# Kernel tuning notes

Measured on AMD Instinct MI355X. Metric: run time of the kernel, lower is better.

The kernel has to match this reference:

```python
import jax, jax.numpy as jnp
import numpy as np

D_MODEL = 256
D_STATE = 64
NGROUPS = 2
EXPAND = 4
HEADDIM = 128
D_CONV = 4
D_INNER = EXPAND * D_MODEL              # 1024
NHEADS = D_INNER // HEADDIM             # 8
GN = NGROUPS * D_STATE                  # 128
D_IN_PROJ = 2 * D_INNER + 2 * GN + NHEADS  # 2312
EPS = 1e-5


def setup_inputs() -> dict:
    key = jax.random.key(0)
    ks = jax.random.split(key, 12)
    B, L = 2, 4096
    u = jax.random.normal(ks[0], (B, L, D_MODEL), dtype=jnp.float32)
    ln_gamma = jnp.ones((D_MODEL,), jnp.float32)
    ln_beta = jnp.zeros((D_MODEL,), jnp.float32)
    W_in = jax.random.normal(ks[1], (D_MODEL, D_IN_PROJ), jnp.float32) / np.sqrt(D_MODEL)
    conv_w = jax.random.normal(ks[2], (D_INNER + 2 * GN, D_CONV), jnp.float32) * 0.2
    conv_b = jax.random.normal(ks[3], (D_INNER + 2 * GN,), jnp.float32) * 0.02
    dt_bias = jnp.log(jnp.expm1(jax.random.uniform(ks[4], (NHEADS,), jnp.float32, 0.001, 0.1)))
    A_log = jnp.log(jax.random.uniform(ks[5], (NHEADS,), jnp.float32, 1.0, 16.0))
    D_param = jnp.ones((NHEADS,), jnp.float32)
    B_head_scale = jnp.ones((NHEADS, GN), jnp.float32) + 0.02 * jax.random.normal(ks[6], (NHEADS, GN), jnp.float32)
    rms_weight = jnp.ones((D_INNER,), jnp.float32)
    W_out = jax.random.normal(ks[7], (D_INNER, D_MODEL), jnp.float32) / np.sqrt(D_INNER)
    return dict(u=u, ln_gamma=ln_gamma, ln_beta=ln_beta, W_in=W_in, conv_w=conv_w,
                conv_b=conv_b, dt_bias=dt_bias, A_log=A_log, D_param=D_param,
                B_head_scale=B_head_scale, rms_weight=rms_weight, W_out=W_out)


def _mamba_mes(xn, W_in, conv_w, conv_b, dt_bias, A_log, D_param, B_head_scale, rms_weight, W_out):
    B, L, _ = xn.shape
    H, P, K = NHEADS, HEADDIM, D_CONV
    zxbcdt = xn @ W_in                                   # (B,L,2312)
    z = zxbcdt[..., :D_INNER]
    xBC = zxbcdt[..., D_INNER:D_INNER + D_INNER + 2 * GN]
    dt = zxbcdt[..., -H:]
    dt_pos = jax.nn.softplus(dt + dt_bias)               # (B,L,H)
    # causal depthwise conv1d + silu
    xp = jnp.pad(xBC, ((0, 0), (K - 1, 0), (0, 0)))
    conv = sum(xp[:, k:k + L, :] * conv_w[:, k] for k in range(K)) + conv_b
    xBC = jax.nn.silu(conv)
    x = xBC[..., :D_INNER]
    B_shared = xBC[..., D_INNER:D_INNER + GN]            # (B,L,GN)
    C_shared = xBC[..., D_INNER + GN:]                   # (B,L,GN)
    # MES: per-head B via diagonal scale, shared x (mean over heads) and shared C
    B_h = B_shared[:, :, None, :] * B_head_scale[None, None]          # (B,L,H,GN)
    x_shared = x.reshape(B, L, H, P).mean(axis=2)                     # (B,L,P)
    A = -jnp.exp(A_log)                                               # (H,)
    dA = jnp.exp(dt_pos * A)                                          # (B,L,H)
    # selective scan; per-head state (GN, P)
    def step(state, inp):
        dA_t, dt_t, B_t, C_t, x_t = inp   # (B,H),(B,H),(B,H,GN),(B,GN),(B,P)
        state = dA_t[:, :, None, None] * state + jnp.einsum('bh,bhn,bp->bhnp', dt_t, B_t, x_t)
        y_t = jnp.einsum('bn,bhnp->bhp', C_t, state)
        return state, y_t
    init = jnp.zeros((B, H, GN, P), xn.dtype)
    xs = (jnp.moveaxis(dA, 1, 0), jnp.moveaxis(dt_pos, 1, 0), jnp.moveaxis(B_h, 1, 0),
          jnp.moveaxis(C_shared, 1, 0), jnp.moveaxis(x_shared, 1, 0))
    _, ys = jax.lax.scan(step, init, xs)
    y = jnp.moveaxis(ys, 0, 1)                                        # (B,L,H,P)
    y = y + D_param[None, None, :, None] * x_shared[:, :, None, :]    # skip term D*x
    y = y.reshape(B, L, D_INNER)
    # gated RMSNorm: y * silu(z), then rmsnorm
    yg = y * jax.nn.silu(z)
    y = yg * jax.lax.rsqrt(jnp.mean(yg * yg, axis=-1, keepdims=True) + EPS) * rms_weight
    return y @ W_out


def reference(u, ln_gamma, ln_beta, W_in, conv_w, conv_b, dt_bias, A_log,
              D_param, B_head_scale, rms_weight, W_out):
    # pre-LayerNorm
    mu = jnp.mean(u, axis=-1, keepdims=True)
    var = jnp.mean((u - mu) ** 2, axis=-1, keepdims=True)
    xn = (u - mu) * jax.lax.rsqrt(var + EPS) * ln_gamma + ln_beta
    out = _mamba_mes(xn, W_in, conv_w, conv_b, dt_bias, A_log, D_param,
                     B_head_scale, rms_weight, W_out)
    return u + out  # dropout is identity in eval
```

## Files before the change

### kernel.cpp

```cpp
#include <hip/hip_runtime.h>
#include <math.h>

#define LN_TOK 4096
#define NB 2
#define NROWS (NB * LN_TOK)
#define DMODEL 256
#define DINNER 1024
#define NHEADS 8
#define GNN 128
#define DPROJ 2312
#define ZSTRIDE 2432
#define EPSF 1e-5f
#define NCHUNK 32
#define CHUNK 128
#define APAD 72
#define BPAD 64
#define MPAD 136
#define TT 16

typedef unsigned short u16;
typedef unsigned int u32;
typedef __attribute__((ext_vector_type(8))) short shortx8;
typedef __attribute__((ext_vector_type(4))) float floatx4;

__device__ __forceinline__ float sigmoidf_(float v) { return 1.f / (1.f + __expf(-v)); }
__device__ __forceinline__ float siluf_(float v)    { return v / (1.f + __expf(-v)); }
__device__ __forceinline__ float softplusf_(float v){ return v > 20.f ? v : log1pf(__expf(v)); }
__device__ __forceinline__ float b2f(u16 h) { return __uint_as_float(((u32)h) << 16); }
__device__ __forceinline__ u16 f2b(float f) {
    u32 u = __float_as_uint(f);
    u32 r = (u + 0x7fffu + ((u >> 16) & 1u)) >> 16;
    return (u16)r;
}
__device__ __forceinline__ void gld16(const void* g, void* l) {
    __builtin_amdgcn_global_load_lds((const __attribute__((address_space(1))) unsigned int*)g,
                                     (__attribute__((address_space(3))) unsigned int*)l, 16, 0, 0);
}

__global__ __launch_bounds__(256) void k_prologue(const float* __restrict__ u,
                                                  const float* __restrict__ gam,
                                                  const float* __restrict__ bet,
                                                  u16* __restrict__ xn,
                                                  const float* __restrict__ W_in,
                                                  u16* __restrict__ Wt,
                                                  const float* __restrict__ W_out,
                                                  u16* __restrict__ Wot) {
    __shared__ float smem[64 * 65];
    int bid = blockIdx.x;
    int tid = threadIdx.x;
    if (bid < NROWS) {
        float v = u[(size_t)bid * DMODEL + tid];
        float* s1 = smem;
        float* s2 = smem + 256;
        s1[tid] = v; s2[tid] = v * v;
        __syncthreads();
        for (int off = 128; off > 0; off >>= 1) {
            if (tid < off) { s1[tid] += s1[tid + off]; s2[tid] += s2[tid + off]; }
            __syncthreads();
        }
        float mean = s1[0] * (1.f / DMODEL);
        float var  = s2[0] * (1.f / DMODEL) - mean * mean;
        float r = rsqrtf(var + EPSF);
        xn[(size_t)bid * DMODEL + tid] = f2b((v - mean) * r * gam[tid] + bet[tid]);
    } else {
        const float* in; u16* outp; int R, C, Cp, gx, gy;
        if (bid < NROWS + 152) {
            int q = bid - NROWS;
            in = W_in; outp = Wt; R = DMODEL; C = DPROJ; Cp = ZSTRIDE;
            gx = q % (ZSTRIDE / 64); gy = q / (ZSTRIDE / 64);
        } else {
            int q = bid - NROWS - 152;
            in = W_out; outp = Wot; R = DINNER; C = DMODEL; Cp = DMODEL;
            gx = q % (DMODEL / 64); gy = q / (DMODEL / 64);
        }
        float (*tile)[65] = (float(*)[65])smem;
        int c0 = gx * 64, r0 = gy * 64;
        int tx = tid & 63, ty = tid >> 6;
        for (int rr = ty; rr < 64; rr += 4) {
            int r = r0 + rr, c = c0 + tx;
            tile[rr][tx] = (r < R && c < C) ? in[(size_t)r * C + c] : 0.f;
        }
        __syncthreads();
        for (int cc = ty; cc < 64; cc += 4) {
            int c = c0 + cc, r = r0 + tx;
            if (c < Cp && r < R) outp[(size_t)c * R + r] = f2b(tile[tx][cc]);
        }
    }
}

__global__ __launch_bounds__(256) void k_gemm_bf(const u16* __restrict__ A,
                                                 const u16* __restrict__ Bt,
                                                 u16* __restrict__ C,
                                                 int K, int ldc) {
    __shared__ u16 As[128 * BPAD];
    __shared__ u16 Bs[128 * BPAD];
    int tid = threadIdx.x;
    int wave = tid >> 6, lane = tid & 63;
    int wm = wave >> 1, wn = wave & 1;
    int quad = lane >> 4, l16 = lane & 15;
    int m0 = blockIdx.y * 128, n0 = blockIdx.x * 128;
    floatx4 acc[4][4] = {};
    for (int k0 = 0; k0 < K; k0 += 64) {
#pragma unroll
        for (int p = 0; p < 4; p++) {
            int i = p * 256 + tid;
            int row = i >> 3, kk = (i & 7) << 3;
            gld16(&A[(size_t)(m0 + row) * K + k0 + kk], &As[i * 8]);
            gld16(&Bt[(size_t)(n0 + row) * K + k0 + kk], &Bs[i * 8]);
        }
        __syncthreads();
#pragma unroll
        for (int ks = 0; ks < 64; ks += 32) {
            shortx8 af[4], bfr[4];
#pragma unroll
            for (int i = 0; i < 4; i++)
                af[i] = *(shortx8*)&As[(wm * 64 + i * 16 + l16) * BPAD + ks + (quad << 3)];
#pragma unroll
            for (int j = 0; j < 4; j++)
                bfr[j] = *(shortx8*)&Bs[(wn * 64 + j * 16 + l16) * BPAD + ks + (quad << 3)];
#pragma unroll
            for (int i = 0; i < 4; i++)
#pragma unroll
                for (int j = 0; j < 4; j++)
                    acc[i][j] = __builtin_amdgcn_mfma_f32_16x16x32_bf16(af[i], bfr[j], acc[i][j], 0, 0, 0);
        }
        __syncthreads();
    }
#pragma unroll
    for (int i = 0; i < 4; i++) {
        int row = m0 + wm * 64 + i * 16 + quad * 4;
#pragma unroll
        for (int j = 0; j < 4; j++) {
            int col = n0 + wn * 64 + j * 16 + l16;
#pragma unroll
            for (int r = 0; r < 4; r++)
                C[(size_t)(row + r) * ldc + col] = f2b(acc[i][j][r]);
        }
    }
}

__global__ __launch_bounds__(256) void k_gemm2(const u16* __restrict__ A,
                                               const u16* __restrict__ Bt,
                                               float* __restrict__ C,
                                               int K, int ldc,
                                               const float* __restrict__ addC) {
    __shared__ u16 As[128 * BPAD];
    __shared__ u16 Bs[64 * BPAD];
    int tid = threadIdx.x;
    int wave = tid >> 6, lane = tid & 63;
    int wm = wave >> 1, wn = wave & 1;
    int quad = lane >> 4, l16 = lane & 15;
    int m0 = blockIdx.y * 128, n0 = blockIdx.x * 64;
    floatx4 acc[4][2] = {};
    for (int k0 = 0; k0 < K; k0 += 64) {
#pragma unroll
        for (int p = 0; p < 4; p++) {
            int i = p * 256 + tid;
            int row = i >> 3, kk = (i & 7) << 3;
            gld16(&A[(size_t)(m0 + row) * K + k0 + kk], &As[i * 8]);
        }
#pragma unroll
        for (int p = 0; p < 2; p++) {
            int i = p * 256 + tid;
            int row = i >> 3, kk = (i & 7) << 3;
            gld16(&Bt[(size_t)(n0 + row) * K + k0 + kk], &Bs[i * 8]);
        }
        __syncthreads();
#pragma unroll
        for (int ks = 0; ks < 64; ks += 32) {
            shortx8 af[4], bfr[2];
#pragma unroll
            for (int i = 0; i < 4; i++)
                af[i] = *(shortx8*)&As[(wm * 64 + i * 16 + l16) * BPAD + ks + (quad << 3)];
#pragma unroll
            for (int j = 0; j < 2; j++)
                bfr[j] = *(shortx8*)&Bs[(wn * 32 + j * 16 + l16) * BPAD + ks + (quad << 3)];
#pragma unroll
            for (int i = 0; i < 4; i++)
#pragma unroll
                for (int j = 0; j < 2; j++)
                    acc[i][j] = __builtin_amdgcn_mfma_f32_16x16x32_bf16(af[i], bfr[j], acc[i][j], 0, 0, 0);
        }
        __syncthreads();
    }
#pragma unroll
    for (int i = 0; i < 4; i++) {
        int row = m0 + wm * 64 + i * 16 + quad * 4;
#pragma unroll
        for (int j = 0; j < 2; j++) {
            int col = n0 + wn * 32 + j * 16 + l16;
#pragma unroll
            for (int r = 0; r < 4; r++) {
                size_t idx = (size_t)(row + r) * ldc + col;
                float v = acc[i][j][r];
                if (addC) v += addC[idx];
                C[idx] = v;
            }
        }
    }
}

#define LDW 1296
__global__ __launch_bounds__(256) void k_conv(const u16* __restrict__ zxb,
                                              const float* __restrict__ cw,
                                              const float* __restrict__ cb,
                                              const float* __restrict__ dt_bias,
                                              const float* __restrict__ A_log,
                                              u16* __restrict__ xsh, u16* __restrict__ Bsh,
                                              u16* __restrict__ Csh, u16* __restrict__ XT,
                                              u16* __restrict__ BT,
                                              float* __restrict__ dtp, float* __restrict__ laa) {
    int blk = blockIdx.x;
    int b = blk / (LN_TOK / TT), tile = blk % (LN_TOK / TT);
    int t0 = tile * TT;
    int tid = threadIdx.x;
    __shared__ u16 ld[(TT + 3) * LDW];
    __shared__ float sv[TT][260];
    __shared__ u16 bcv[TT][132];

    for (int i = tid; i < (TT + 3) * 161; i += 256) {
        int r = i / 161, ch = (i % 161) * 8;
        int t = t0 - 3 + r;
        int4 v = make_int4(0, 0, 0, 0);
        if (t >= 0)
            v = *(const int4*)&zxb[((size_t)(b * LN_TOK + t)) * ZSTRIDE + DINNER + ch];
        *(int4*)&ld[r * LDW + ch] = v;
    }

    int cmap[5];
#pragma unroll
    for (int k = 0; k < 4; k++) cmap[k] = (tid >> 7) * 512 + (tid & 127) + 128 * k;
    cmap[4] = 1024 + tid;
    float w0[5], w1[5], w2[5], w3[5], bias[5];
#pragma unroll
    for (int k = 0; k < 5; k++) {
        int c = cmap[k];
        w0[k] = cw[c * 4 + 0]; w1[k] = cw[c * 4 + 1];
        w2[k] = cw[c * 4 + 2]; w3[k] = cw[c * 4 + 3];
        bias[k] = cb[c];
    }
    float dtb = 0.f, negA = 0.f;
    if (tid < NHEADS) { dtb = dt_bias[tid]; negA = -__expf(A_log[tid]); }

    __syncthreads();

    float h1[5], h2[5], h3[5];
#pragma unroll
    for (int k = 0; k < 5; k++) {
        h3[k] = b2f(ld[0 * LDW + cmap[k]]);
        h2[k] = b2f(ld[1 * LDW + cmap[k]]);
        h1[k] = b2f(ld[2 * LDW + cmap[k]]);
    }

    for (int m = 0; m < TT; m++) {
        int t = t0 + m;
        size_t rowp = (size_t)(b * LN_TOK + t) * GNN;
        float xpart = 0.f;
#pragma unroll
        for (int k = 0; k < 5; k++) {
            float cur = b2f(ld[(m + 3) * LDW + cmap[k]]);
            float conv = bias[k] + w3[k] * cur + w2[k] * h1[k] + w1[k] * h2[k] + w0[k] * h3[k];
            h3[k] = h2[k]; h2[k] = h1[k]; h1[k] = cur;
            float s = siluf_(conv);
            if (k < 4) xpart += s;
            else {
                u16 sb = f2b(s);
                if (tid < 128) { Bsh[rowp + tid] = sb; bcv[m][tid] = sb; }
                else           Csh[rowp + tid - 128] = sb;
            }
        }
        sv[m][tid] = xpart;
        if (tid < NHEADS) {
            float dtv = b2f(ld[(m + 3) * LDW + 1280 + tid]) + dtb;
            float dp = softplusf_(dtv);
            size_t idx = ((size_t)(b * NHEADS + tid)) * LN_TOK + t;
            dtp[idx] = dp;
            laa[idx] = negA * dp;
        }
    }
    __syncthreads();

    for (int idx = tid; idx < TT * 128; idx += 256) {
        int m = idx >> 7, p = idx & 127;
        xsh[(size_t)(b * LN_TOK + t0 + m) * GNN + p] =
            f2b((sv[m][p] + sv[m][p + 128]) * 0.125f);
    }
    {
        int p = tid & 127, tg = tid >> 7;
        u16 ox[8], ob[8];
#pragma unroll
        for (int j = 0; j < 8; j++) {
            int m = tg * 8 + j;
            ox[j] = f2b((sv[m][p] + sv[m][p + 128]) * 0.125f);
            ob[j] = bcv[m][p];
        }
        size_t base = ((size_t)(b * GNN + p)) * LN_TOK + t0 + tg * 8;
        int4 vx = make_int4((u32)ox[0] | ((u32)ox[1] << 16), (u32)ox[2] | ((u32)ox[3] << 16),
                            (u32)ox[4] | ((u32)ox[5] << 16), (u32)ox[6] | ((u32)ox[7] << 16));
        int4 vb = make_int4((u32)ob[0] | ((u32)ob[1] << 16), (u32)ob[2] | ((u32)ob[3] << 16),
                            (u32)ob[4] | ((u32)ob[5] << 16), (u32)ob[6] | ((u32)ob[7] << 16));
        *(int4*)&XT[base] = vx;
        *(int4*)&BT[base] = vb;
    }
}

__global__ __launch_bounds__(256) void k_chunkS(const u16* __restrict__ BT,
                                                const u16* __restrict__ XT,
                                                const float* __restrict__ scale,
                                                const float* __restrict__ laa,
                                                const float* __restrict__ dtp,
                                                u16* __restrict__ states,
                                                float* __restrict__ gtot) {
    int blk = blockIdx.x;
    int c = blk & 31, h = (blk >> 5) & 7, b = blk >> 8;
    int t0 = c * CHUNK;
    __shared__ u16 As[128 * APAD];
    __shared__ u16 Bs[128 * APAD];
    __shared__ float g[128], esc[128], scl[128];
    int tid = threadIdx.x;
    int wave = tid >> 6, lane = tid & 63;
    int wm = wave >> 1, wn = wave & 1;
    int quad = lane >> 4, l16 = lane & 15;
    size_t bhbase = (size_t)(b * NHEADS + h) * LN_TOK + t0;
    if (tid < 128) g[tid] = laa[bhbase + tid];
    __syncthreads();
#pragma unroll
    for (int off = 1; off < 128; off <<= 1) {
        float v = 0.f;
        if (tid < 128 && tid >= off) v = g[tid - off];
        __syncthreads();
        if (tid < 128) g[tid] += v;
        __syncthreads();
    }
    if (tid < 128) {
        esc[tid] = __expf(g[127] - g[tid]) * dtp[bhbase + tid];
        scl[tid] = scale[h * GNN + tid];
    }
    if (tid == 0) gtot[(size_t)(b * NHEADS + h) * NCHUNK + c] = g[127];
    __syncthreads();
    floatx4 acc[4][4] = {};
    size_t tbase = (size_t)(b * GNN) * LN_TOK + t0;
    for (int k0 = 0; k0 < 128; k0 += 64) {
#pragma unroll
        for (int p = 0; p < 4; p++) {
            int i = p * 256 + tid;
            int row = i >> 3, kk = (i & 7) << 3;
            int4 raw = *(const int4*)&BT[tbase + (size_t)row * LN_TOK + k0 + kk];
            u16* rp = (u16*)&raw;
            float sr = scl[row];
            u32 w[4];
#pragma unroll
            for (int q = 0; q < 4; q++) {
                u16 a  = f2b(b2f(rp[2 * q])     * sr * esc[k0 + kk + 2 * q]);
                u16 bb = f2b(b2f(rp[2 * q + 1]) * sr * esc[k0 + kk + 2 * q + 1]);
                w[q] = (u32)a | ((u32)bb << 16);
            }
            *(int4*)&As[row * APAD + kk] = make_int4(w[0], w[1], w[2], w[3]);
            *(int4*)&Bs[row * APAD + kk] = *(const int4*)&XT[tbase + (size_t)row * LN_TOK + k0 + kk];
        }
        __syncthreads();
#pragma unroll
        for (int ks = 0; ks < 64; ks += 32) {
            shortx8 af[4], bfr[4];
#pragma unroll
            for (int i = 0; i < 4; i++)
                af[i] = *(shortx8*)&As[(wm * 64 + i * 16 + l16) * APAD + ks + (quad << 3)];
#pragma unroll
            for (int j = 0; j < 4; j++)
                bfr[j] = *(shortx8*)&Bs[(wn * 64 + j * 16 + l16) * APAD + ks + (quad << 3)];
#pragma unroll
            for (int i = 0; i < 4; i++)
#pragma unroll
                for (int j = 0; j < 4; j++)
                    acc[i][j] = __builtin_amdgcn_mfma_f32_16x16x32_bf16(af[i], bfr[j], acc[i][j], 0, 0, 0);
        }
        __syncthreads();
    }
    size_t sbase = (size_t)blk * 16384;
#pragma unroll
    for (int i = 0; i < 4; i++) {
        int n0 = wm * 64 + i * 16 + quad * 4;
#pragma unroll
        for (int j = 0; j < 4; j++) {
            int p = wn * 64 + j * 16 + l16;
            u16 o[4];
#pragma unroll
            for (int r = 0; r < 4; r++) o[r] = f2b(acc[i][j][r]);
            u32 lo = (u32)o[0] | ((u32)o[1] << 16);
            u32 hi = (u32)o[2] | ((u32)o[3] << 16);
            *(uint2*)&states[sbase + (size_t)p * CHUNK + n0] = make_uint2(lo, hi);
        }
    }
}

__global__ void k_scan(u16* __restrict__ states, const float* __restrict__ gtot) {
    int idx = blockIdx.x * 256 + threadIdx.x;
    int bh = idx >> 13;
    int np = (idx & 8191) * 2;
    __shared__ float sG[NCHUNK];
    if (threadIdx.x < NCHUNK) sG[threadIdx.x] = __expf(gtot[bh * NCHUNK + threadIdx.x]);
    __syncthreads();
    size_t base = (size_t)bh * NCHUNK * 16384 + np;
    float r0 = 0.f, r1 = 0.f;
    u32 v = *(u32*)&states[base];
    for (int c = 0; c < NCHUNK; c++) {
        u32 vn = (c < NCHUNK - 1) ? *(u32*)&states[base + (size_t)(c + 1) * 16384] : 0u;
        float l0 = b2f((u16)(v & 0xffff)), l1 = b2f((u16)(v >> 16));
        *(u32*)&states[base + (size_t)c * 16384] = (u32)f2b(r0) | ((u32)f2b(r1) << 16);
        float G = sG[c];
        r0 = G * r0 + l0; r1 = G * r1 + l1;
        v = vn;
    }
}

__global__ __launch_bounds__(256) void k_chunkMY(const u16* __restrict__ Bsh,
                                                 const u16* __restrict__ Csh,
                                                 const float* __restrict__ scale,
                                                 const u16* __restrict__ states,
                                                 const u16* __restrict__ XT,
                                                 const float* __restrict__ laa,
                                                 const float* __restrict__ dtp,
                                                 u16* __restrict__ y) {
    int blk = blockIdx.x;
    int c = blk & 31, h = (blk >> 5) & 7, b = blk >> 8;
    int t0 = c * CHUNK;
    __shared__ u16 As[128 * APAD];
    __shared__ u16 Bs[128 * APAD];
    __shared__ u16 Mt[128 * MPAD];
    __shared__ float g[128], dts[128], sc[128], eg[128];
    int tid = threadIdx.x;
    int wave = tid >> 6, lane = tid & 63;
    int wm = wave >> 1, wn = wave & 1;
    int quad = lane >> 4, l16 = lane & 15;
    size_t bhbase = (size_t)(b * NHEADS + h) * LN_TOK + t0;
    if (tid < 128) g[tid] = laa[bhbase + tid];
    __syncthreads();
#pragma unroll
    for (int off = 1; off < 128; off <<= 1) {
        float v = 0.f;
        if (tid < 128 && tid >= off) v = g[tid - off];
        __syncthreads();
        if (tid < 128) g[tid] += v;
        __syncthreads();
    }
    if (tid < 128) {
        eg[tid] = __expf(g[tid]);
        dts[tid] = dtp[bhbase + tid];
        sc[tid] = scale[h * GNN + tid];
    }
    __syncthreads();
    floatx4 acc[4][4] = {};
    size_t rbase = (size_t)(b * LN_TOK + t0) * GNN;
    for (int k0 = 0; k0 < 128; k0 += 64) {
#pragma unroll
        for (int p = 0; p < 4; p++) {
            int i = p * 256 + tid;
            int row = i >> 3, kk = (i & 7) << 3;
            int4 raw = *(const int4*)&Bsh[rbase + (size_t)row * GNN + k0 + kk];
            u16* rp = (u16*)&raw;
            u32 w[4];
#pragma unroll
            for (int q = 0; q < 4; q++) {
                u16 a  = f2b(b2f(rp[2 * q])     * sc[k0 + kk + 2 * q]);
                u16 bb = f2b(b2f(rp[2 * q + 1]) * sc[k0 + kk + 2 * q + 1]);
                w[q] = (u32)a | ((u32)bb << 16);
            }
            *(int4*)&As[row * APAD + kk] = make_int4(w[0], w[1], w[2], w[3]);
            *(int4*)&Bs[row * APAD + kk] = *(const int4*)&Csh[rbase + (size_t)row * GNN + k0 + kk];
        }
        __syncthreads();
#pragma unroll
        for (int ks = 0; ks < 64; ks += 32) {
            shortx8 af[4], bfr[4];
#pragma unroll
            for (int i = 0; i < 4; i++)
                af[i] = *(shortx8*)&As[(wm * 64 + i * 16 + l16) * APAD + ks + (quad << 3)];
#pragma unroll
            for (int j = 0; j < 4; j++)
                bfr[j] = *(shortx8*)&Bs[(wn * 64 + j * 16 + l16) * APAD + ks + (quad << 3)];
#pragma unroll
            for (int i = 0; i < 4; i++)
#pragma unroll
                for (int j = 0; j < 4; j++)
                    acc[i][j] = __builtin_amdgcn_mfma_f32_16x16x32_bf16(af[i], bfr[j], acc[i][j], 0, 0, 0);
        }
        __syncthreads();
    }
#pragma unroll
    for (int i = 0; i < 4; i++) {
        int s0 = wm * 64 + i * 16 + quad * 4;
#pragma unroll
        for (int j = 0; j < 4; j++) {
            int t = wn * 64 + j * 16 + l16;
            u16 o[4];
#pragma unroll
            for (int r = 0; r < 4; r++) {
                int s = s0 + r;
                float v = (s <= t) ? acc[i][j][r] * __expf(g[t] - g[s]) * dts[s] : 0.f;
                o[r] = f2b(v);
            }
            u32 lo = (u32)o[0] | ((u32)o[1] << 16);
            u32 hi = (u32)o[2] | ((u32)o[3] << 16);
            *(uint2*)&Mt[t * MPAD + s0] = make_uint2(lo, hi);
            acc[i][j] = (floatx4){0.f, 0.f, 0.f, 0.f};
        }
    }
    __syncthreads();
    size_t sbase = (size_t)blk * 16384;
    for (int k0 = 0; k0 < 128; k0 += 64) {
#pragma unroll
        for (int p = 0; p < 4; p++) {
            int i = p * 256 + tid;
            int row = i >> 3, kk = (i & 7) << 3;
            int4 raw = *(const int4*)&Csh[rbase + (size_t)row * GNN + k0 + kk];
            float e = eg[row];
            u16* rp = (u16*)&raw;
            u32 w[4];
#pragma unroll
            for (int q = 0; q < 4; q++) {
                u16 a  = f2b(b2f(rp[2 * q]) * e);
                u16 bb = f2b(b2f(rp[2 * q + 1]) * e);
                w[q] = (u32)a | ((u32)bb << 16);
            }
            *(int4*)&As[row * APAD + kk] = make_int4(w[0], w[1], w[2], w[3]);
            *(int4*)&Bs[row * APAD + kk] = *(const int4*)&states[sbase + (size_t)row * CHUNK + k0 + kk];
        }
        __syncthreads();
#pragma unroll
        for (int ks = 0; ks < 64; ks += 32) {
            shortx8 af[4], bfr[4];
#pragma unroll
            for (int i = 0; i < 4; i++)
                af[i] = *(shortx8*)&As[(wm * 64 + i * 16 + l16) * APAD + ks + (quad << 3)];
#pragma unroll
            for (int j = 0; j < 4; j++)
                bfr[j] = *(shortx8*)&Bs[(wn * 64 + j * 16 + l16) * APAD + ks + (quad << 3)];
#pragma unroll
            for (int i = 0; i < 4; i++)
#pragma unroll
                for (int j = 0; j < 4; j++)
                    acc[i][j] = __builtin_amdgcn_mfma_f32_16x16x32_bf16(af[i], bfr[j], acc[i][j], 0, 0, 0);
        }
        __syncthreads();
    }
    size_t xtb = (size_t)(b * GNN) * LN_TOK + t0;
    for (int k0 = 0; k0 < 128; k0 += 64) {
#pragma unroll
        for (int p = 0; p < 4; p++) {
            int i = p * 256 + tid;
            int row = i >> 3, kk = (i & 7) << 3;
            *(int4*)&Bs[row * APAD + kk] = *(const int4*)&XT[xtb + (size_t)row * LN_TOK + k0 + kk];
        }
        __syncthreads();
#pragma unroll
        for (int ks = 0; ks < 64; ks += 32) {
            shortx8 af[4], bfr[4];
#pragma unroll
            for (int i = 0; i < 4; i++)
                af[i] = *(shortx8*)&Mt[(wm * 64 + i * 16 + l16) * MPAD + k0 + ks + (quad << 3)];
#pragma unroll
            for (int j = 0; j < 4; j++)
                bfr[j] = *(shortx8*)&Bs[(wn * 64 + j * 16 + l16) * APAD + ks + (quad << 3)];
#pragma unroll
            for (int i = 0; i < 4; i++)
#pragma unroll
                for (int j = 0; j < 4; j++)
                    acc[i][j] = __builtin_amdgcn_mfma_f32_16x16x32_bf16(af[i], bfr[j], acc[i][j], 0, 0, 0);
        }
        __syncthreads();
    }
#pragma unroll
    for (int i = 0; i < 4; i++) {
        int t = wm * 64 + i * 16 + quad * 4;
#pragma unroll
        for (int j = 0; j < 4; j++) {
            int p = wn * 64 + j * 16 + l16;
#pragma unroll
            for (int r = 0; r < 4; r++)
                y[((size_t)(b * LN_TOK + t0 + t + r)) * DINNER + h * GNN + p] = f2b(acc[i][j][r]);
        }
    }
}

__global__ void k_gate(const u16* __restrict__ y, const u16* __restrict__ zxb,
                       const u16* __restrict__ xsh, const float* __restrict__ Dp,
                       const float* __restrict__ rw, u16* __restrict__ ybuf) {
    int row = blockIdx.x;
    int tid = threadIdx.x;
    size_t yb = (size_t)row * DINNER;
    size_t zb = (size_t)row * ZSTRIDE;
    size_t xb = (size_t)row * GNN;
    float yg[4];
    float ss = 0.f;
#pragma unroll
    for (int q = 0; q < 4; q++) {
        int k = tid * 4 + q;
        int h = k >> 7, p = k & 127;
        float z = b2f(zxb[zb + k]);
        float v = (b2f(y[yb + k]) + Dp[h] * b2f(xsh[xb + p])) * z * sigmoidf_(z);
        yg[q] = v;
        ss += v * v;
    }
    __shared__ float red[256];
    red[tid] = ss;
    __syncthreads();
    for (int off = 128; off > 0; off >>= 1) {
        if (tid < off) red[tid] += red[tid + off];
        __syncthreads();
    }
    float scale = rsqrtf(red[0] * (1.f / DINNER) + EPSF);
#pragma unroll
    for (int q = 0; q < 4; q++) {
        int k = tid * 4 + q;
        ybuf[yb + k] = f2b(yg[q] * scale * rw[k]);
    }
}

extern "C" void kernel_launch(void* const* d_in, const int* in_sizes, int n_in,
                              void* d_out, int out_size, void* d_ws, size_t ws_size,
                              hipStream_t stream) {
    (void)in_sizes; (void)n_in; (void)out_size; (void)ws_size;
    const float* u        = (const float*)d_in[0];
    const float* ln_gamma = (const float*)d_in[1];
    const float* ln_beta  = (const float*)d_in[2];
    const float* W_in     = (const float*)d_in[3];
    const float* conv_w   = (const float*)d_in[4];
    const float* conv_b   = (const float*)d_in[5];
    const float* dt_bias  = (const float*)d_in[6];
    const float* A_log    = (const float*)d_in[7];
    const float* D_param  = (const float*)d_in[8];
    const float* B_scale  = (const float*)d_in[9];
    const float* rms_w    = (const float*)d_in[10];
    const float* W_out    = (const float*)d_in[11];
    float* out = (float*)d_out;

    char* ws = (char*)d_ws;
    u16*   xn_b   = (u16*)ws;                 ws += (size_t)NROWS * DMODEL * 2;
    u16*   Wt     = (u16*)ws;                 ws += (size_t)ZSTRIDE * DMODEL * 2;
    u16*   Wot    = (u16*)ws;                 ws += (size_t)DMODEL * DINNER * 2;
    u16*   zxb    = (u16*)ws;                 ws += (size_t)NROWS * ZSTRIDE * 2;
    u16*   xsh    = (u16*)ws;                 ws += (size_t)NROWS * GNN * 2;
    u16*   Bsh    = (u16*)ws;                 ws += (size_t)NROWS * GNN * 2;
    u16*   Csh    = (u16*)ws;                 ws += (size_t)NROWS * GNN * 2;
    u16*   XT     = (u16*)ws;                 ws += (size_t)NB * GNN * LN_TOK * 2;
    u16*   BT     = (u16*)ws;                 ws += (size_t)NB * GNN * LN_TOK * 2;
    float* dtp    = (float*)ws;               ws += (size_t)NB * NHEADS * LN_TOK * 4;
    float* laa    = (float*)ws;               ws += (size_t)NB * NHEADS * LN_TOK * 4;
    float* gtot   = (float*)ws;               ws += (size_t)NB * NHEADS * NCHUNK * 4;
    u16*   states = (u16*)ws;                 ws += (size_t)512 * 16384 * 2;
    u16*   ybig   = (u16*)ws;                 ws += (size_t)NROWS * DINNER * 2;
    u16*   ybuf   = (u16*)ws;                 ws += (size_t)NROWS * DINNER * 2;

    k_prologue<<<NROWS + 152 + 64, 256, 0, stream>>>(u, ln_gamma, ln_beta, xn_b,
                                                     W_in, Wt, W_out, Wot);

    k_gemm_bf<<<dim3(ZSTRIDE / 128, NROWS / 128), 256, 0, stream>>>(xn_b, Wt, zxb, DMODEL, ZSTRIDE);

    k_conv<<<NROWS / TT, 256, 0, stream>>>(zxb, conv_w, conv_b, dt_bias, A_log,
                                           xsh, Bsh, Csh, XT, BT, dtp, laa);

    k_chunkS<<<NB * NHEADS * NCHUNK, 256, 0, stream>>>(BT, XT, B_scale, laa, dtp, states, gtot);

    k_scan<<<512, 256, 0, stream>>>(states, gtot);

    k_chunkMY<<<NB * NHEADS * NCHUNK, 256, 0, stream>>>(Bsh, Csh, B_scale, states, XT,
                                                        laa, dtp, ybig);

    k_gate<<<NROWS, 256, 0, stream>>>(ybig, zxb, xsh, D_param, rms_w, ybuf);

    k_gemm2<<<dim3(DMODEL / 64, NROWS / 128), 256, 0, stream>>>(ybuf, Wot, out, DINNER, DMODEL, u);
}
```

Measured before the change: 212.0 us.

## Fuse chunk-state, scan and chunk-output kernels into one cooperative kernel

Merges the three SSM stages (per-chunk state GEMM, inter-chunk scan, output GEMMs) into a single cooperative kernel that uses grid-wide syncs instead of separate launches. This keeps laa prefix sums and scale values in shared memory across stages and drops two launch boundaries. It also merges the Mt and A shared buffers and reorders the intra-chunk MY GEMM ahead of the state contribution. If the cooperative launch fails it falls back to the three-kernel path. Grid syncs across 512 blocks require all blocks to be co-resident and can add their own latency.

```diff
diff --git a/kernel.cpp b/kernel.cpp
--- a/kernel.cpp
+++ b/kernel.cpp
@@ -1,4 +1,5 @@
 #include <hip/hip_runtime.h>
+#include <hip/hip_cooperative_groups.h>
 #include <math.h>
 
 #define LN_TOK 4096
@@ -413,38 +414,37 @@
     }
 }
 
-__global__ __launch_bounds__(256) void k_chunkMY(const u16* __restrict__ Bsh,
-                                                 const u16* __restrict__ Csh,
-                                                 const float* __restrict__ scale,
-                                                 const u16* __restrict__ states,
-                                                 const u16* __restrict__ XT,
-                                                 const float* __restrict__ laa,
-                                                 const float* __restrict__ dtp,
-                                                 u16* __restrict__ y) {
+__global__ __launch_bounds__(256) void k_chunkMY2(const u16* __restrict__ Bsh,
+                                                  const u16* __restrict__ Csh,
+                                                  const float* __restrict__ scale,
+                                                  const u16* __restrict__ states,
+                                                  const u16* __restrict__ XT,
+                                                  const float* __restrict__ laa,
+                                                  const float* __restrict__ dtp,
+                                                  u16* __restrict__ y) {
     int blk = blockIdx.x;
     int c = blk & 31, h = (blk >> 5) & 7, b = blk >> 8;
     int t0 = c * CHUNK;
-    __shared__ u16 As[128 * APAD];
+    __shared__ u16 MtAs[128 * MPAD];
     __shared__ u16 Bs[128 * APAD];
-    __shared__ u16 Mt[128 * MPAD];
-    __shared__ float g[128], dts[128], sc[128], eg[128];
+    __shared__ float gsh[128], eg[128], dts[128], sc[128];
     int tid = threadIdx.x;
     int wave = tid >> 6, lane = tid & 63;
     int wm = wave >> 1, wn = wave & 1;
     int quad = lane >> 4, l16 = lane & 15;
     size_t bhbase = (size_t)(b * NHEADS + h) * LN_TOK + t0;
-    if (tid < 128) g[tid] = laa[bhbase + tid];
+    if (tid < 128) gsh[tid] = laa[bhbase + tid];
     __syncthreads();
 #pragma unroll
     for (int off = 1; off < 128; off <<= 1) {
         float v = 0.f;
-        if (tid < 128 && tid >= off) v = g[tid - off];
-        __syncthreads();
-        if (tid < 128) g[tid] += v;
+        if (tid < 128 && tid >= off) v = gsh[tid - off];
+        __syncthreads();
+        if (tid < 128) gsh[tid] += v;
         __syncthreads();
     }
     if (tid < 128) {
-        eg[tid] = __expf(g[tid]);
+        eg[tid] = __expf(gsh[tid]);
         dts[tid] = dtp[bhbase + tid];
         sc[tid] = scale[h * GNN + tid];
     }
@@ -465,7 +465,7 @@
                 u16 bb = f2b(b2f(rp[2 * q + 1]) * sc[k0 + kk + 2 * q + 1]);
                 w[q] = (u32)a | ((u32)bb << 16);
             }
-            *(int4*)&As[row * APAD + kk] = make_int4(w[0], w[1], w[2], w[3]);
+            *(int4*)&MtAs[row * APAD + kk] = make_int4(w[0], w[1], w[2], w[3]);
             *(int4*)&Bs[row * APAD + kk] = *(const int4*)&Csh[rbase + (size_t)row * GNN + k0 + kk];
         }
         __syncthreads();
@@ -474,7 +474,7 @@
             shortx8 af[4], bfr[4];
 #pragma unroll
             for (int i = 0; i < 4; i++)
-                af[i] = *(shortx8*)&As[(wm * 64 + i * 16 + l16) * APAD + ks + (quad << 3)];
+                af[i] = *(shortx8*)&MtAs[(wm * 64 + i * 16 + l16) * APAD + ks + (quad << 3)];
 #pragma unroll
             for (int j = 0; j < 4; j++)
                 bfr[j] = *(shortx8*)&Bs[(wn * 64 + j * 16 + l16) * APAD + ks + (quad << 3)];
@@ -496,16 +496,42 @@
 #pragma unroll
             for (int r = 0; r < 4; r++) {
                 int s = s0 + r;
-                float v = (s <= t) ? acc[i][j][r] * __expf(g[t] - g[s]) * dts[s] : 0.f;
+                float v = (s <= t) ? acc[i][j][r] * __expf(gsh[t] - gsh[s]) * dts[s] : 0.f;
                 o[r] = f2b(v);
             }
             u32 lo = (u32)o[0] | ((u32)o[1] << 16);
             u32 hi = (u32)o[2] | ((u32)o[3] << 16);
-            *(uint2*)&Mt[t * MPAD + s0] = make_uint2(lo, hi);
+            *(uint2*)&MtAs[t * MPAD + s0] = make_uint2(lo, hi);
             acc[i][j] = (floatx4){0.f, 0.f, 0.f, 0.f};
         }
     }
     __syncthreads();
+    size_t xtb = (size_t)(b * GNN) * LN_TOK + t0;
+    for (int k0 = 0; k0 < 128; k0 += 64) {
+#pragma unroll
+        for (int p = 0; p < 4; p++) {
+            int i = p * 256 + tid;
+            int row = i >> 3, kk = (i & 7) << 3;
+            *(int4*)&Bs[row * APAD + kk] = *(const int4*)&XT[xtb + (size_t)row * LN_TOK + k0 + kk];
+        }
+        __syncthreads();
+#pragma unroll
+        for (int ks = 0; ks < 64; ks += 32) {
+            shortx8 af[4], bfr[4];
+#pragma unroll
+            for (int i = 0; i < 4; i++)
+                af[i] = *(shortx8*)&MtAs[(wm * 64 + i * 16 + l16) * MPAD + k0 + ks + (quad << 3)];
+#pragma unroll
+            for (int j = 0; j < 4; j++)
+                bfr[j] = *(shortx8*)&Bs[(wn * 64 + j * 16 + l16) * APAD + ks + (quad << 3)];
+#pragma unroll
+            for (int i = 0; i < 4; i++)
+#pragma unroll
+                for (int j = 0; j < 4; j++)
+                    acc[i][j] = __builtin_amdgcn_mfma_f32_16x16x32_bf16(af[i], bfr[j], acc[i][j], 0, 0, 0);
+        }
+        __syncthreads();
+    }
     size_t sbase = (size_t)blk * 16384;
     for (int k0 = 0; k0 < 128; k0 += 64) {
 #pragma unroll
@@ -522,7 +548,7 @@
                 u16 bb = f2b(b2f(rp[2 * q + 1]) * e);
                 w[q] = (u32)a | ((u32)bb << 16);
             }
-            *(int4*)&As[row * APAD + kk] = make_int4(w[0], w[1], w[2], w[3]);
+            *(int4*)&MtAs[row * APAD + kk] = make_int4(w[0], w[1], w[2], w[3]);
             *(int4*)&Bs[row * APAD + kk] = *(const int4*)&states[sbase + (size_t)row * CHUNK + k0 + kk];
         }
         __syncthreads();
@@ -531,7 +557,7 @@
             shortx8 af[4], bfr[4];
 #pragma unroll
             for (int i = 0; i < 4; i++)
-                af[i] = *(shortx8*)&As[(wm * 64 + i * 16 + l16) * APAD + ks + (quad << 3)];
+                af[i] = *(shortx8*)&MtAs[(wm * 64 + i * 16 + l16) * APAD + ks + (quad << 3)];
 #pragma unroll
             for (int j = 0; j < 4; j++)
                 bfr[j] = *(shortx8*)&Bs[(wn * 64 + j * 16 + l16) * APAD + ks + (quad << 3)];
@@ -543,6 +569,202 @@
         }
         __syncthreads();
     }
+#pragma unroll
+    for (int i = 0; i < 4; i++) {
+        int t = wm * 64 + i * 16 + quad * 4;
+#pragma unroll
+        for (int j = 0; j < 4; j++) {
+            int p = wn * 64 + j * 16 + l16;
+#pragma unroll
+            for (int r = 0; r < 4; r++)
+                y[((size_t)(b * LN_TOK + t0 + t + r)) * DINNER + h * GNN + p] = f2b(acc[i][j][r]);
+        }
+    }
+}
+
+__global__ __launch_bounds__(256, 2) void k_ssm(const u16* __restrict__ BT,
+                                                const u16* __restrict__ XT,
+                                                const float* __restrict__ scale,
+                                                const float* __restrict__ laa,
+                                                const float* __restrict__ dtp,
+                                                u16* __restrict__ states,
+                                                float* __restrict__ gtot,
+                                                const u16* __restrict__ Bsh,
+                                                const u16* __restrict__ Csh,
+                                                u16* __restrict__ y) {
+    cooperative_groups::grid_group gg = cooperative_groups::this_grid();
+    __shared__ u16 MtAs[128 * MPAD];
+    __shared__ u16 Bs[128 * APAD];
+    __shared__ float gsh[128];
+    __shared__ float aux[128];
+    __shared__ float dts[128], sc[128];
+    int blk = blockIdx.x;
+    int c = blk & 31, h = (blk >> 5) & 7, b = blk >> 8;
+    int t0 = c * CHUNK;
+    int tid = threadIdx.x;
+    int wave = tid >> 6, lane = tid & 63;
+    int wm = wave >> 1, wn = wave & 1;
+    int quad = lane >> 4, l16 = lane & 15;
+    size_t bhbase = (size_t)(b * NHEADS + h) * LN_TOK + t0;
+
+    if (tid < 128) gsh[tid] = laa[bhbase + tid];
+    __syncthreads();
+#pragma unroll
+    for (int off = 1; off < 128; off <<= 1) {
+        float v = 0.f;
+        if (tid < 128 && tid >= off) v = gsh[tid - off];
+        __syncthreads();
+        if (tid < 128) gsh[tid] += v;
+        __syncthreads();
+    }
+    if (tid < 128) {
+        aux[tid] = __expf(gsh[127] - gsh[tid]) * dtp[bhbase + tid];
+        sc[tid] = scale[h * GNN + tid];
+    }
+    if (tid == 0) gtot[(size_t)(b * NHEADS + h) * NCHUNK + c] = gsh[127];
+    __syncthreads();
+
+    {
+        floatx4 acc[4][4] = {};
+        size_t tbase = (size_t)(b * GNN) * LN_TOK + t0;
+        for (int k0 = 0; k0 < 128; k0 += 64) {
+#pragma unroll
+            for (int p = 0; p < 4; p++) {
+                int i = p * 256 + tid;
+                int row = i >> 3, kk = (i & 7) << 3;
+                int4 raw = *(const int4*)&BT[tbase + (size_t)row * LN_TOK + k0 + kk];
+                u16* rp = (u16*)&raw;
+                float sr = sc[row];
+                u32 w[4];
+#pragma unroll
+                for (int q = 0; q < 4; q++) {
+                    u16 a  = f2b(b2f(rp[2 * q])     * sr * aux[k0 + kk + 2 * q]);
+                    u16 bb = f2b(b2f(rp[2 * q + 1]) * sr * aux[k0 + kk + 2 * q + 1]);
+                    w[q] = (u32)a | ((u32)bb << 16);
+                }
+                *(int4*)&MtAs[row * APAD + kk] = make_int4(w[0], w[1], w[2], w[3]);
+                *(int4*)&Bs[row * APAD + kk] = *(const int4*)&XT[tbase + (size_t)row * LN_TOK + k0 + kk];
+            }
+            __syncthreads();
+#pragma unroll
+            for (int ks = 0; ks < 64; ks += 32) {
+                shortx8 af[4], bfr[4];
+#pragma unroll
+                for (int i = 0; i < 4; i++)
+                    af[i] = *(shortx8*)&MtAs[(wm * 64 + i * 16 + l16) * APAD + ks + (quad << 3)];
+#pragma unroll
+                for (int j = 0; j < 4; j++)
+                    bfr[j] = *(shortx8*)&Bs[(wn * 64 + j * 16 + l16) * APAD + ks + (quad << 3)];
+#pragma unroll
+                for (int i = 0; i < 4; i++)
+#pragma unroll
+                    for (int j = 0; j < 4; j++)
+                        acc[i][j] = __builtin_amdgcn_mfma_f32_16x16x32_bf16(af[i], bfr[j], acc[i][j], 0, 0, 0);
+            }
+            __syncthreads();
+        }
+        size_t sbase = (size_t)blk * 16384;
+#pragma unroll
+        for (int i = 0; i < 4; i++) {
+            int n0 = wm * 64 + i * 16 + quad * 4;
+#pragma unroll
+            for (int j = 0; j < 4; j++) {
+                int p = wn * 64 + j * 16 + l16;
+                u16 o[4];
+#pragma unroll
+                for (int r = 0; r < 4; r++) o[r] = f2b(acc[i][j][r]);
+                u32 lo = (u32)o[0] | ((u32)o[1] << 16);
+                u32 hi = (u32)o[2] | ((u32)o[3] << 16);
+                *(uint2*)&states[sbase + (size_t)p * CHUNK + n0] = make_uint2(lo, hi);
+            }
+        }
+    }
+
+    gg.sync();
+
+    {
+        int idx = blk * 256 + tid;
+        int bh2 = idx >> 13;
+        int np = (idx & 8191) * 2;
+        if (tid < NCHUNK) aux[tid] = __expf(gtot[bh2 * NCHUNK + tid]);
+        __syncthreads();
+        size_t base = (size_t)bh2 * NCHUNK * 16384 + np;
+        float r0 = 0.f, r1 = 0.f;
+        u32 v = *(u32*)&states[base];
+        for (int cc = 0; cc < NCHUNK; cc++) {
+            u32 vn = (cc < NCHUNK - 1) ? *(u32*)&states[base + (size_t)(cc + 1) * 16384] : 0u;
+            float l0 = b2f((u16)(v & 0xffff)), l1 = b2f((u16)(v >> 16));
+            *(u32*)&states[base + (size_t)cc * 16384] = (u32)f2b(r0) | ((u32)f2b(r1) << 16);
+            float G = aux[cc];
+            r0 = G * r0 + l0; r1 = G * r1 + l1;
+            v = vn;
+        }
+    }
+
+    gg.sync();
+
+    if (tid < 128) {
+        aux[tid] = __expf(gsh[tid]);
+        dts[tid] = dtp[bhbase + tid];
+    }
+    __syncthreads();
+    floatx4 acc[4][4] = {};
+    size_t rbase = (size_t)(b * LN_TOK + t0) * GNN;
+    for (int k0 = 0; k0 < 128; k0 += 64) {
+#pragma unroll
+        for (int p = 0; p < 4; p++) {
+            int i = p * 256 + tid;
+            int row = i >> 3, kk = (i & 7) << 3;
+            int4 raw = *(const int4*)&Bsh[rbase + (size_t)row * GNN + k0 + kk];
+            u16* rp = (u16*)&raw;
+            u32 w[4];
+#pragma unroll
+            for (int q = 0; q < 4; q++) {
+                u16 a  = f2b(b2f(rp[2 * q])     * sc[k0 + kk + 2 * q]);
+                u16 bb = f2b(b2f(rp[2 * q + 1]) * sc[k0 + kk + 2 * q + 1]);
+                w[q] = (u32)a | ((u32)bb << 16);
+            }
+            *(int4*)&MtAs[row * APAD + kk] = make_int4(w[0], w[1], w[2], w[3]);
+            *(int4*)&Bs[row * APAD + kk] = *(const int4*)&Csh[rbase + (size_t)row * GNN + k0 + kk];
+        }
+        __syncthreads();
+#pragma unroll
+        for (int ks = 0; ks < 64; ks += 32) {
+            shortx8 af[4], bfr[4];
+#pragma unroll
+            for (int i = 0; i < 4; i++)
+                af[i] = *(shortx8*)&MtAs[(wm * 64 + i * 16 + l16) * APAD + ks + (quad << 3)];
+#pragma unroll
+            for (int j = 0; j < 4; j++)
+                bfr[j] = *(shortx8*)&Bs[(wn * 64 + j * 16 + l16) * APAD + ks + (quad << 3)];
+#pragma unroll
+            for (int i = 0; i < 4; i++)
+#pragma unroll
+                for (int j = 0; j < 4; j++)
+                    acc[i][j] = __builtin_amdgcn_mfma_f32_16x16x32_bf16(af[i], bfr[j], acc[i][j], 0, 0, 0);
+        }
+        __syncthreads();
+    }
+#pragma unroll
+    for (int i = 0; i < 4; i++) {
+        int s0 = wm * 64 + i * 16 + quad * 4;
+#pragma unroll
+        for (int j = 0; j < 4; j++) {
+            int t = wn * 64 + j * 16 + l16;
+            u16 o[4];
+#pragma unroll
+            for (int r = 0; r < 4; r++) {
+                int s = s0 + r;
+                float v = (s <= t) ? acc[i][j][r] * __expf(gsh[t] - gsh[s]) * dts[s] : 0.f;
+                o[r] = f2b(v);
+            }
+            u32 lo = (u32)o[0] | ((u32)o[1] << 16);
+            u32 hi = (u32)o[2] | ((u32)o[3] << 16);
+            *(uint2*)&MtAs[t * MPAD + s0] = make_uint2(lo, hi);
+            acc[i][j] = (floatx4){0.f, 0.f, 0.f, 0.f};
+        }
+    }
+    __syncthreads();
     size_t xtb = (size_t)(b * GNN) * LN_TOK + t0;
     for (int k0 = 0; k0 < 128; k0 += 64) {
 #pragma unroll
@@ -557,7 +779,44 @@
             shortx8 af[4], bfr[4];
 #pragma unroll
             for (int i = 0; i < 4; i++)
-                af[i] = *(shortx8*)&Mt[(wm * 64 + i * 16 + l16) * MPAD + k0 + ks + (quad << 3)];
+                af[i] = *(shortx8*)&MtAs[(wm * 64 + i * 16 + l16) * MPAD + k0 + ks + (quad << 3)];
+#pragma unroll
+            for (int j = 0; j < 4; j++)
+                bfr[j] = *(shortx8*)&Bs[(wn * 64 + j * 16 + l16) * APAD + ks + (quad << 3)];
+#pragma unroll
+            for (int i = 0; i < 4; i++)
+#pragma unroll
+                for (int j = 0; j < 4; j++)
+                    acc[i][j] = __builtin_amdgcn_mfma_f32_16x16x32_bf16(af[i], bfr[j], acc[i][j], 0, 0, 0);
+        }
+        __syncthreads();
+    }
+    size_t sbase = (size_t)blk * 16384;
+    for (int k0 = 0; k0 < 128; k0 += 64) {
+#pragma unroll
+        for (int p = 0; p < 4; p++) {
+            int i = p * 256 + tid;
+            int row = i >> 3, kk = (i & 7) << 3;
+            int4 raw = *(const int4*)&Csh[rbase + (size_t)row * GNN + k0 + kk];
+            float e = aux[row];
+            u16* rp = (u16*)&raw;
+            u32 w[4];
+#pragma unroll
+            for (int q = 0; q < 4; q++) {
+                u16 a  = f2b(b2f(rp[2 * q]) * e);
+                u16 bb = f2b(b2f(rp[2 * q + 1]) * e);
+                w[q] = (u32)a | ((u32)bb << 16);
+            }
+            *(int4*)&MtAs[row * APAD + kk] = make_int4(w[0], w[1], w[2], w[3]);
+            *(int4*)&Bs[row * APAD + kk] = *(const int4*)&states[sbase + (size_t)row * CHUNK + k0 + kk];
+        }
+        __syncthreads();
+#pragma unroll
+        for (int ks = 0; ks < 64; ks += 32) {
+            shortx8 af[4], bfr[4];
+#pragma unroll
+            for (int i = 0; i < 4; i++)
+                af[i] = *(shortx8*)&MtAs[(wm * 64 + i * 16 + l16) * APAD + ks + (quad << 3)];
 #pragma unroll
             for (int j = 0; j < 4; j++)
                 bfr[j] = *(shortx8*)&Bs[(wn * 64 + j * 16 + l16) * APAD + ks + (quad << 3)];
@@ -659,12 +918,22 @@
     k_conv<<<NROWS / TT, 256, 0, stream>>>(zxb, conv_w, conv_b, dt_bias, A_log,
                                            xsh, Bsh, Csh, XT, BT, dtp, laa);
 
-    k_chunkS<<<NB * NHEADS * NCHUNK, 256, 0, stream>>>(BT, XT, B_scale, laa, dtp, states, gtot);
-
-    k_scan<<<512, 256, 0, stream>>>(states, gtot);
-
-    k_chunkMY<<<NB * NHEADS * NCHUNK, 256, 0, stream>>>(Bsh, Csh, B_scale, states, XT,
-                                                        laa, dtp, ybig);
+    {
+        void* cargs[] = { (void*)&BT, (void*)&XT, (void*)&B_scale, (void*)&laa,
+                          (void*)&dtp, (void*)&states, (void*)&gtot,
+                          (void*)&Bsh, (void*)&Csh, (void*)&ybig };
+        hipError_t e = hipLaunchCooperativeKernel((const void*)k_ssm,
+                                                  dim3(NB * NHEADS * NCHUNK),
+                                                  dim3(256), cargs, 0, stream);
+        if (e != hipSuccess) {
+            (void)hipGetLastError();
+            k_chunkS<<<NB * NHEADS * NCHUNK, 256, 0, stream>>>(BT, XT, B_scale, laa, dtp,
+                                                               states, gtot);
+            k_scan<<<512, 256, 0, stream>>>(states, gtot);
+            k_chunkMY2<<<NB * NHEADS * NCHUNK, 256, 0, stream>>>(Bsh, Csh, B_scale, states,
+                                                                 XT, laa, dtp, ybig);
+        }
+    }
 
     k_gate<<<NROWS, 256, 0, stream>>>(ybig, zxb, xsh, D_param, rms_w, ybuf);
 
```

Result: slower. 360.7 us (+70.1%).

## Load chunk GEMM B operands directly to LDS and alias Mt with A tile

Applied to the files above, without the earlier changes.

In both chunk kernels, the B-operand tiles (XT, Csh, states) are now copied from global memory straight into unpadded LDS with gld16, instead of passing through registers with a padded stride. In k_chunkMY2 the intra-chunk Mt@X product now runs before the C@states product, so the A tile can share storage with Mt and total LDS per block shrinks. This is meant to cut register staging and instruction overhead and to allow more resident blocks. The unpadded BPAD layout risks LDS bank conflicts on the fragment reads.

```diff
diff --git a/kernel.cpp b/kernel.cpp
--- a/kernel.cpp
+++ b/kernel.cpp
@@ -315,7 +315,7 @@
     int c = blk & 31, h = (blk >> 5) & 7, b = blk >> 8;
     int t0 = c * CHUNK;
     __shared__ u16 As[128 * APAD];
-    __shared__ u16 Bs[128 * APAD];
+    __shared__ u16 Bs[128 * BPAD];
     __shared__ float g[128], esc[128], scl[128];
     int tid = threadIdx.x;
     int wave = tid >> 6, lane = tid & 63;
@@ -345,6 +345,7 @@
         for (int p = 0; p < 4; p++) {
             int i = p * 256 + tid;
             int row = i >> 3, kk = (i & 7) << 3;
+            gld16(&XT[tbase + (size_t)row * LN_TOK + k0 + kk], &Bs[i * 8]);
             int4 raw = *(const int4*)&BT[tbase + (size_t)row * LN_TOK + k0 + kk];
             u16* rp = (u16*)&raw;
             float sr = scl[row];
@@ -356,7 +357,6 @@
                 w[q] = (u32)a | ((u32)bb << 16);
             }
             *(int4*)&As[row * APAD + kk] = make_int4(w[0], w[1], w[2], w[3]);
-            *(int4*)&Bs[row * APAD + kk] = *(const int4*)&XT[tbase + (size_t)row * LN_TOK + k0 + kk];
         }
         __syncthreads();
 #pragma unroll
@@ -367,7 +367,7 @@
                 af[i] = *(shortx8*)&As[(wm * 64 + i * 16 + l16) * APAD + ks + (quad << 3)];
 #pragma unroll
             for (int j = 0; j < 4; j++)
-                bfr[j] = *(shortx8*)&Bs[(wn * 64 + j * 16 + l16) * APAD + ks + (quad << 3)];
+                bfr[j] = *(shortx8*)&Bs[(wn * 64 + j * 16 + l16) * BPAD + ks + (quad << 3)];
 #pragma unroll
             for (int i = 0; i < 4; i++)
 #pragma unroll
@@ -413,38 +413,37 @@
     }
 }
 
-__global__ __launch_bounds__(256) void k_chunkMY(const u16* __restrict__ Bsh,
-                                                 const u16* __restrict__ Csh,
-                                                 const float* __restrict__ scale,
-                                                 const u16* __restrict__ states,
-                                                 const u16* __restrict__ XT,
-                                                 const float* __restrict__ laa,
-                                                 const float* __restrict__ dtp,
-                                                 u16* __restrict__ y) {
+__global__ __launch_bounds__(256) void k_chunkMY2(const u16* __restrict__ Bsh,
+                                                  const u16* __restrict__ Csh,
+                                                  const float* __restrict__ scale,
+                                                  const u16* __restrict__ states,
+                                                  const u16* __restrict__ XT,
+                                                  const float* __restrict__ laa,
+                                                  const float* __restrict__ dtp,
+                                                  u16* __restrict__ y) {
     int blk = blockIdx.x;
     int c = blk & 31, h = (blk >> 5) & 7, b = blk >> 8;
     int t0 = c * CHUNK;
-    __shared__ u16 As[128 * APAD];
-    __shared__ u16 Bs[128 * APAD];
-    __shared__ u16 Mt[128 * MPAD];
-    __shared__ float g[128], dts[128], sc[128], eg[128];
+    __shared__ u16 MtAs[128 * MPAD];
+    __shared__ u16 Bs[128 * BPAD];
+    __shared__ float gsh[128], eg[128], dts[128], sc[128];
     int tid = threadIdx.x;
     int wave = tid >> 6, lane = tid & 63;
     int wm = wave >> 1, wn = wave & 1;
     int quad = lane >> 4, l16 = lane & 15;
     size_t bhbase = (size_t)(b * NHEADS + h) * LN_TOK + t0;
-    if (tid < 128) g[tid] = laa[bhbase + tid];
+    if (tid < 128) gsh[tid] = laa[bhbase + tid];
     __syncthreads();
 #pragma unroll
     for (int off = 1; off < 128; off <<= 1) {
         float v = 0.f;
-        if (tid < 128 && tid >= off) v = g[tid - off];
-        __syncthreads();
-        if (tid < 128) g[tid] += v;
+        if (tid < 128 && tid >= off) v = gsh[tid - off];
+        __syncthreads();
+        if (tid < 128) gsh[tid] += v;
         __syncthreads();
     }
     if (tid < 128) {
-        eg[tid] = __expf(g[tid]);
+        eg[tid] = __expf(gsh[tid]);
         dts[tid] = dtp[bhbase + tid];
         sc[tid] = scale[h * GNN + tid];
     }
@@ -456,6 +455,7 @@
         for (int p = 0; p < 4; p++) {
             int i = p * 256 + tid;
             int row = i >> 3, kk = (i & 7) << 3;
+            gld16(&Csh[rbase + (size_t)row * GNN + k0 + kk], &Bs[i * 8]);
             int4 raw = *(const int4*)&Bsh[rbase + (size_t)row * GNN + k0 + kk];
             u16* rp = (u16*)&raw;
             u32 w[4];
@@ -465,8 +465,7 @@
                 u16 bb = f2b(b2f(rp[2 * q + 1]) * sc[k0 + kk + 2 * q + 1]);
                 w[q] = (u32)a | ((u32)bb << 16);
             }
-            *(int4*)&As[row * APAD + kk] = make_int4(w[0], w[1], w[2], w[3]);
-            *(int4*)&Bs[row * APAD + kk] = *(const int4*)&Csh[rbase + (size_t)row * GNN + k0 + kk];
+            *(int4*)&MtAs[row * APAD + kk] = make_int4(w[0], w[1], w[2], w[3]);
         }
         __syncthreads();
 #pragma unroll
@@ -474,10 +473,10 @@
             shortx8 af[4], bfr[4];
 #pragma unroll
             for (int i = 0; i < 4; i++)
-                af[i] = *(shortx8*)&As[(wm * 64 + i * 16 + l16) * APAD + ks + (quad << 3)];
+                af[i] = *(shortx8*)&MtAs[(wm * 64 + i * 16 + l16) * APAD + ks + (quad << 3)];
 #pragma unroll
             for (int j = 0; j < 4; j++)
-                bfr[j] = *(shortx8*)&Bs[(wn * 64 + j * 16 + l16) * APAD + ks + (quad << 3)];
+                bfr[j] = *(shortx8*)&Bs[(wn * 64 + j * 16 + l16) * BPAD + ks + (quad << 3)];
 #pragma unroll
             for (int i = 0; i < 4; i++)
 #pragma unroll
@@ -496,22 +495,49 @@
 #pragma unroll
             for (int r = 0; r < 4; r++) {
                 int s = s0 + r;
-                float v = (s <= t) ? acc[i][j][r] * __expf(g[t] - g[s]) * dts[s] : 0.f;
+                float v = (s <= t) ? acc[i][j][r] * __expf(gsh[t] - gsh[s]) * dts[s] : 0.f;
                 o[r] = f2b(v);
             }
             u32 lo = (u32)o[0] | ((u32)o[1] << 16);
             u32 hi = (u32)o[2] | ((u32)o[3] << 16);
-            *(uint2*)&Mt[t * MPAD + s0] = make_uint2(lo, hi);
+            *(uint2*)&MtAs[t * MPAD + s0] = make_uint2(lo, hi);
             acc[i][j] = (floatx4){0.f, 0.f, 0.f, 0.f};
         }
     }
     __syncthreads();
-    size_t sbase = (size_t)blk * 16384;
+    size_t xtb = (size_t)(b * GNN) * LN_TOK + t0;
     for (int k0 = 0; k0 < 128; k0 += 64) {
 #pragma unroll
         for (int p = 0; p < 4; p++) {
             int i = p * 256 + tid;
             int row = i >> 3, kk = (i & 7) << 3;
+            gld16(&XT[xtb + (size_t)row * LN_TOK + k0 + kk], &Bs[i * 8]);
+        }
+        __syncthreads();
+#pragma unroll
+        for (int ks = 0; ks < 64; ks += 32) {
+            shortx8 af[4], bfr[4];
+#pragma unroll
+            for (int i = 0; i < 4; i++)
+                af[i] = *(shortx8*)&MtAs[(wm * 64 + i * 16 + l16) * MPAD + k0 + ks + (quad << 3)];
+#pragma unroll
+            for (int j = 0; j < 4; j++)
+                bfr[j] = *(shortx8*)&Bs[(wn * 64 + j * 16 + l16) * BPAD + ks + (quad << 3)];
+#pragma unroll
+            for (int i = 0; i < 4; i++)
+#pragma unroll
+                for (int j = 0; j < 4; j++)
+                    acc[i][j] = __builtin_amdgcn_mfma_f32_16x16x32_bf16(af[i], bfr[j], acc[i][j], 0, 0, 0);
+        }
+        __syncthreads();
+    }
+    size_t sbase = (size_t)blk * 16384;
+    for (int k0 = 0; k0 < 128; k0 += 64) {
+#pragma unroll
+        for (int p = 0; p < 4; p++) {
+            int i = p * 256 + tid;
+            int row = i >> 3, kk = (i & 7) << 3;
+            gld16(&states[sbase + (size_t)row * CHUNK + k0 + kk], &Bs[i * 8]);
             int4 raw = *(const int4*)&Csh[rbase + (size_t)row * GNN + k0 + kk];
             float e = eg[row];
             u16* rp = (u16*)&raw;
@@ -522,8 +548,7 @@
                 u16 bb = f2b(b2f(rp[2 * q + 1]) * e);
                 w[q] = (u32)a | ((u32)bb << 16);
             }
-            *(int4*)&As[row * APAD + kk] = make_int4(w[0], w[1], w[2], w[3]);
-            *(int4*)&Bs[row * APAD + kk] = *(const int4*)&states[sbase + (size_t)row * CHUNK + k0 + kk];
+            *(int4*)&MtAs[row * APAD + kk] = make_int4(w[0], w[1], w[2], w[3]);
         }
         __syncthreads();
 #pragma unroll
@@ -531,36 +556,10 @@
             shortx8 af[4], bfr[4];
 #pragma unroll
             for (int i = 0; i < 4; i++)
-                af[i] = *(shortx8*)&As[(wm * 64 + i * 16 + l16) * APAD + ks + (quad << 3)];
+                af[i] = *(shortx8*)&MtAs[(wm * 64 + i * 16 + l16) * APAD + ks + (quad << 3)];
 #pragma unroll
             for (int j = 0; j < 4; j++)
-                bfr[j] = *(shortx8*)&Bs[(wn * 64 + j * 16 + l16) * APAD + ks + (quad << 3)];
-#pragma unroll
-            for (int i = 0; i < 4; i++)
-#pragma unroll
-                for (int j = 0; j < 4; j++)
-                    acc[i][j] = __builtin_amdgcn_mfma_f32_16x16x32_bf16(af[i], bfr[j], acc[i][j], 0, 0, 0);
-        }
-        __syncthreads();
-    }
-    size_t xtb = (size_t)(b * GNN) * LN_TOK + t0;
-    for (int k0 = 0; k0 < 128; k0 += 64) {
-#pragma unroll
-        for (int p = 0; p < 4; p++) {
-            int i = p * 256 + tid;
-            int row = i >> 3, kk = (i & 7) << 3;
-            *(int4*)&Bs[row * APAD + kk] = *(const int4*)&XT[xtb + (size_t)row * LN_TOK + k0 + kk];
-        }
-        __syncthreads();
-#pragma unroll
-        for (int ks = 0; ks < 64; ks += 32) {
-            shortx8 af[4], bfr[4];
-#pragma unroll
-            for (int i = 0; i < 4; i++)
-                af[i] = *(shortx8*)&Mt[(wm * 64 + i * 16 + l16) * MPAD + k0 + ks + (quad << 3)];
-#pragma unroll
-            for (int j = 0; j < 4; j++)
-                bfr[j] = *(shortx8*)&Bs[(wn * 64 + j * 16 + l16) * APAD + ks + (quad << 3)];
+                bfr[j] = *(shortx8*)&Bs[(wn * 64 + j * 16 + l16) * BPAD + ks + (quad << 3)];
 #pragma unroll
             for (int i = 0; i < 4; i++)
 #pragma unroll
@@ -663,8 +662,8 @@
 
     k_scan<<<512, 256, 0, stream>>>(states, gtot);
 
-    k_chunkMY<<<NB * NHEADS * NCHUNK, 256, 0, stream>>>(Bsh, Csh, B_scale, states, XT,
-                                                        laa, dtp, ybig);
+    k_chunkMY2<<<NB * NHEADS * NCHUNK, 256, 0, stream>>>(Bsh, Csh, B_scale, states,
+                                                         XT, laa, dtp, ybig);
 
     k_gate<<<NROWS, 256, 0, stream>>>(ybig, zxb, xsh, D_param, rms_w, ybuf);
 
```

Measured after the change: 215.0 us. Within noise of the previous version (+1.4%).
